# Optimization experiments

Measured on AMD Instinct MI355X. Metric: run time of the kernel, lower is better.

## Reference

```python
import jax, jax.numpy as jnp
import numpy as np

B, C, P, H, W = 64, 2048, 4, 14, 14
HID = C * P // 2  # 4096
S = H * W         # 196


def setup_inputs() -> dict:
    key = jax.random.key(0)
    k1, k2, k3, k4, k5 = jax.random.split(key, 5)
    x = jax.random.normal(k1, (B, C, H, W), dtype=jnp.float32)
    w1 = jax.random.normal(k2, (HID, C), dtype=jnp.float32) * 0.02
    b1 = jnp.zeros((HID,), dtype=jnp.float32)
    w2 = jax.random.normal(k3, (C * P, HID), dtype=jnp.float32) * 0.02
    b2 = jnp.zeros((C * P,), dtype=jnp.float32)
    return {"x": x, "w1": w1, "b1": b1, "w2": w2, "b2": b2}


def reference(x, w1, b1, w2, b2):
    # SE-style gating: global average pool -> fc1 -> sigmoid -> fc2 -> sigmoid
    g = x.mean(axis=(2, 3))                                  # [B, C]
    h = jax.nn.sigmoid(g @ w1.T + b1)                        # [B, HID]
    w = jax.nn.sigmoid(h @ w2.T + b2).reshape(B, P, C)       # grouping_result [B, P, C]
    # Weighted feature: mean over channels of w[b,p,c] * x[b,c,s].
    # Original materializes [B,P,C,196] then AdaptiveAvgPool3d over C;
    # mathematically this is a batched matmul divided by C.
    xs = x.reshape(B, C, S)                                  # [B, C, 196]
    feat = jnp.einsum('bpc,bcs->bps', w, xs) / C             # [B, P, 196]
    return (w, feat.reshape(B, P, H, W))
```

## Files before the change

kernel.cpp:

```cpp
#include <hip/hip_runtime.h>
#include <cstdint>
#include <cstddef>

typedef __attribute__((ext_vector_type(4))) float  f32x4;
typedef __attribute__((ext_vector_type(8))) short  short8;
typedef __attribute__((ext_vector_type(4))) short  short4v;

__device__ __forceinline__ short f2bf(float f) {
  unsigned u = __float_as_uint(f);
  u += 0x7FFF + ((u >> 16) & 1);
  return (short)(u >> 16);
}
__device__ __forceinline__ float sigmoidf(float x) {
  return 1.0f / (1.0f + __expf(-x));
}

__global__ __launch_bounds__(256) void pool_kernel(const float* __restrict__ x,
                                                   float* __restrict__ g,
                                                   int nrows) {
  int gid  = blockIdx.x * 256 + threadIdx.x;
  int row  = gid >> 6;
  int lane = threadIdx.x & 63;
  if (row >= nrows) return;
  float s = 0.f;
  if (lane < 49) {
    const float4* p = (const float4*)(x + (size_t)row * 196);
    float4 v = p[lane];
    s = v.x + v.y + v.z + v.w;
  }
#pragma unroll
  for (int off = 32; off > 0; off >>= 1) s += __shfl_down(s, off);
  if (lane == 0) g[row] = s * (1.0f / 196.0f);
}

template<int N, int K, int KCHUNK>
__global__ __launch_bounds__(256) void gemm_bt_part(const float* __restrict__ A,
                                                    const float* __restrict__ B,
                                                    float* __restrict__ part) {
  constexpr int BM = 64, BN = 64, BK = 64;
  constexpr int NT = N / BN;
  const int nt = blockIdx.x % NT;
  const int ks = blockIdx.x / NT;
  const int n0 = nt * BN;
  const int k0 = ks * KCHUNK;

  __shared__ short As[BM * BK];
  __shared__ short Bs[BN * BK];

  const int tid  = threadIdx.x;
  const int lane = tid & 63;
  const int wv   = tid >> 6;
  const int wm   = wv >> 1, wn = wv & 1;

  f32x4 acc[2][2] = {};

  for (int t = 0; t < KCHUNK / BK; ++t) {
    const int kt = k0 + t * BK;
    __syncthreads();
#pragma unroll
    for (int i = 0; i < 4; ++i) {
      int f = i * 256 + tid;
      int row = f >> 4, c4 = f & 15;
      float4 v = *(const float4*)(A + (size_t)row * K + kt + c4 * 4);
      short4v sv; sv.x = f2bf(v.x); sv.y = f2bf(v.y); sv.z = f2bf(v.z); sv.w = f2bf(v.w);
      int bo = (c4 * 8) ^ ((row & 7) << 4);
      *(short4v*)(As + row * 64 + (bo >> 1)) = sv;
    }
#pragma unroll
    for (int i = 0; i < 4; ++i) {
      int f = i * 256 + tid;
      int row = f >> 4, c4 = f & 15;
      float4 v = *(const float4*)(B + (size_t)(n0 + row) * K + kt + c4 * 4);
      short4v sv; sv.x = f2bf(v.x); sv.y = f2bf(v.y); sv.z = f2bf(v.z); sv.w = f2bf(v.w);
      int bo = (c4 * 8) ^ ((row & 7) << 4);
      *(short4v*)(Bs + row * 64 + (bo >> 1)) = sv;
    }
    __syncthreads();
#pragma unroll
    for (int kk = 0; kk < 2; ++kk) {
      const int kbyte = kk * 64 + ((lane >> 4) << 4);
      short8 af[2], bf[2];
#pragma unroll
      for (int mi = 0; mi < 2; ++mi) {
        int row = wm * 32 + mi * 16 + (lane & 15);
        int bo  = kbyte ^ ((row & 7) << 4);
        af[mi]  = *(const short8*)(As + row * 64 + (bo >> 1));
      }
#pragma unroll
      for (int ni = 0; ni < 2; ++ni) {
        int row = wn * 32 + ni * 16 + (lane & 15);
        int bo  = kbyte ^ ((row & 7) << 4);
        bf[ni]  = *(const short8*)(Bs + row * 64 + (bo >> 1));
      }
#pragma unroll
      for (int mi = 0; mi < 2; ++mi)
#pragma unroll
        for (int ni = 0; ni < 2; ++ni)
          acc[mi][ni] = __builtin_amdgcn_mfma_f32_16x16x32_bf16(af[mi], bf[ni], acc[mi][ni], 0, 0, 0);
    }
  }
  float* pp = part + (size_t)ks * BM * N;
#pragma unroll
  for (int mi = 0; mi < 2; ++mi)
#pragma unroll
    for (int ni = 0; ni < 2; ++ni)
#pragma unroll
      for (int r = 0; r < 4; ++r) {
        int m = wm * 32 + mi * 16 + ((lane >> 4) << 2) + r;
        int n = n0 + wn * 32 + ni * 16 + (lane & 15);
        pp[(size_t)m * N + n] = acc[mi][ni][r];
      }
}

template<int KS>
__global__ __launch_bounds__(256) void bias_sigmoid_reduce(const float* __restrict__ part,
                                                           const float* __restrict__ bias,
                                                           float* __restrict__ out,
                                                           int MN, int N) {
  int i = blockIdx.x * 256 + threadIdx.x;
  int e = i * 4;
  if (e >= MN) return;
  float4 s = {0.f, 0.f, 0.f, 0.f};
#pragma unroll
  for (int k = 0; k < KS; ++k) {
    float4 v = *(const float4*)(part + (size_t)k * MN + e);
    s.x += v.x; s.y += v.y; s.z += v.z; s.w += v.w;
  }
  float4 b = *(const float4*)(bias + (e % N));
  s.x = sigmoidf(s.x + b.x);
  s.y = sigmoidf(s.y + b.y);
  s.z = sigmoidf(s.z + b.z);
  s.w = sigmoidf(s.w + b.w);
  *(float4*)(out + e) = s;
}

__global__ __launch_bounds__(256) void einsum_fused(const float* __restrict__ x,
                                                    const float* __restrict__ part,
                                                    const float* __restrict__ b2,
                                                    float* __restrict__ wout,
                                                    float* __restrict__ fpart) {
  const int b  = blockIdx.x >> 4;
  const int cc = blockIdx.x & 15;
  __shared__ float gs[4 * 128];
  const int tid = threadIdx.x;
#pragma unroll
  for (int i = 0; i < 2; ++i) {
    int idx = i * 256 + tid;
    int p = idx >> 7, c = idx & 127;
    int n = p * 2048 + cc * 128 + c;
    float s = 0.f;
#pragma unroll
    for (int ks = 0; ks < 8; ++ks)
      s += part[(size_t)ks * 64 * 8192 + (size_t)b * 8192 + n];
    s = sigmoidf(s + b2[n]);
    wout[(size_t)b * 8192 + n] = s;
    gs[idx] = s;
  }
  __syncthreads();
  if (tid < 196) {
    const float* xp = x + (size_t)b * 2048 * 196 + (size_t)cc * 128 * 196 + tid;
    float a0 = 0, a1 = 0, a2 = 0, a3 = 0;
#pragma unroll 8
    for (int c = 0; c < 128; ++c) {
      float xv = xp[(size_t)c * 196];
      a0 += gs[c]        * xv;
      a1 += gs[128 + c]  * xv;
      a2 += gs[256 + c]  * xv;
      a3 += gs[384 + c]  * xv;
    }
    float* fp = fpart + ((size_t)(b * 16 + cc) * 4) * 196 + tid;
    fp[0]   = a0;
    fp[196] = a1;
    fp[392] = a2;
    fp[588] = a3;
  }
}

__global__ __launch_bounds__(256) void feat_reduce(const float* __restrict__ fpart,
                                                   float* __restrict__ feat) {
  int i = blockIdx.x * 256 + threadIdx.x;
  if (i >= 64 * 4 * 196) return;
  int s = i % 196;
  int p = (i / 196) & 3;
  int b = i / 784;
  float sum = 0.f;
#pragma unroll
  for (int cc = 0; cc < 16; ++cc)
    sum += fpart[((size_t)(b * 16 + cc) * 4 + p) * 196 + s];
  feat[i] = sum * (1.0f / 2048.0f);
}

extern "C" void kernel_launch(void* const* d_in, const int* in_sizes, int n_in,
                              void* d_out, int out_size, void* d_ws, size_t ws_size,
                              hipStream_t stream) {
  const float* x  = (const float*)d_in[0];
  const float* w1 = (const float*)d_in[1];
  const float* b1 = (const float*)d_in[2];
  const float* w2 = (const float*)d_in[3];
  const float* b2 = (const float*)d_in[4];
  float* out = (float*)d_out;

  float* g     = (float*)d_ws;
  float* h     = g + 64 * 2048;
  float* part  = h + 64 * 4096;
  float* fpart = part + 4194304;

  float* wout = out;
  float* feat = out + 524288;

  pool_kernel<<<(64 * 2048) / 4, 256, 0, stream>>>(x, g, 64 * 2048);

  gemm_bt_part<4096, 2048, 128><<<(4096 / 64) * 16, 256, 0, stream>>>(g, w1, part);
  bias_sigmoid_reduce<16><<<(64 * 4096 / 4) / 256, 256, 0, stream>>>(part, b1, h, 64 * 4096, 4096);

  gemm_bt_part<8192, 4096, 512><<<(8192 / 64) * 8, 256, 0, stream>>>(h, w2, part);

  einsum_fused<<<64 * 16, 256, 0, stream>>>(x, part, b2, wout, fpart);

  feat_reduce<<<(50176 + 255) / 256, 256, 0, stream>>>(fpart, feat);
}
```

Measured before the change: 108.9 us.

## Replace split-K GEMMs with in-block K-reduction and fused bias-sigmoid epilogue

Replaces the shared-memory-tiled split-K GEMMs, which wrote full partial-sum arrays to global memory, with a kernel in which each 512-thread block owns 16 output columns. Its 8 waves split K, run register-prefetched MFMAs that read weights straight from global, reduce through shared memory and apply bias plus sigmoid in place. This removes the separate bias/sigmoid reduce kernel and the large partial-sum round trips. Pooled and hidden activations are now stored as bf16 to halve their traffic, and the einsum kernel reads the finished gate weights instead of reducing partials. In exchange there is no LDS reuse of A across columns and each block launches larger.

Result: faster. 105.0 us (-3.6%).

```diff
diff --git a/kernel.cpp b/kernel.cpp
--- a/kernel.cpp
+++ b/kernel.cpp
@@ -4,7 +4,6 @@
 
 typedef __attribute__((ext_vector_type(4))) float  f32x4;
 typedef __attribute__((ext_vector_type(8))) short  short8;
-typedef __attribute__((ext_vector_type(4))) short  short4v;
 
 __device__ __forceinline__ short f2bf(float f) {
   unsigned u = __float_as_uint(f);
@@ -16,7 +15,7 @@
 }
 
 __global__ __launch_bounds__(256) void pool_kernel(const float* __restrict__ x,
-                                                   float* __restrict__ g,
+                                                   short* __restrict__ g,
                                                    int nrows) {
   int gid  = blockIdx.x * 256 + threadIdx.x;
   int row  = gid >> 6;
@@ -30,131 +29,102 @@
   }
 #pragma unroll
   for (int off = 32; off > 0; off >>= 1) s += __shfl_down(s, off);
-  if (lane == 0) g[row] = s * (1.0f / 196.0f);
+  if (lane == 0) g[row] = f2bf(s * (1.0f / 196.0f));
 }
 
-template<int N, int K, int KCHUNK>
-__global__ __launch_bounds__(256) void gemm_bt_part(const float* __restrict__ A,
-                                                    const float* __restrict__ B,
-                                                    float* __restrict__ part) {
-  constexpr int BM = 64, BN = 64, BK = 64;
-  constexpr int NT = N / BN;
-  const int nt = blockIdx.x % NT;
-  const int ks = blockIdx.x / NT;
-  const int n0 = nt * BN;
-  const int k0 = ks * KCHUNK;
+template<int N, int K, bool OUT_BF16>
+__global__ __launch_bounds__(512, 4) void gemm_fused(const short* __restrict__ A,
+                                                     const float* __restrict__ B,
+                                                     const float* __restrict__ bias,
+                                                     void* __restrict__ outp) {
+  constexpr int KW = K / 8;
+  constexpr int NK = KW / 32;
+  const int n0  = blockIdx.x * 16;
+  const int tid = threadIdx.x;
+  const int l   = tid & 63;
+  const int wv  = tid >> 6;
+  const int kw0 = wv * KW;
 
-  __shared__ short As[BM * BK];
-  __shared__ short Bs[BN * BK];
+  __shared__ float red[8 * 1024];
 
-  const int tid  = threadIdx.x;
-  const int lane = tid & 63;
-  const int wv   = tid >> 6;
-  const int wm   = wv >> 1, wn = wv & 1;
+  const int ko = (l >> 4) * 8;
+  const float* Bp = B + (size_t)(n0 + (l & 15)) * K + kw0 + ko;
+  const short* Ap = A + (size_t)(l & 15) * K + kw0 + ko;
 
-  f32x4 acc[2][2] = {};
+  f32x4 acc0 = {}, acc1 = {}, acc2 = {}, acc3 = {};
 
-  for (int t = 0; t < KCHUNK / BK; ++t) {
-    const int kt = k0 + t * BK;
-    __syncthreads();
+  float4 bc0 = *(const float4*)(Bp);
+  float4 bc1 = *(const float4*)(Bp + 4);
+  short8 ac0 = *(const short8*)(Ap);
+  short8 ac1 = *(const short8*)(Ap + 16 * K);
+  short8 ac2 = *(const short8*)(Ap + 32 * K);
+  short8 ac3 = *(const short8*)(Ap + 48 * K);
+
+  for (int t = 0; t < NK; ++t) {
+    float4 bn0 = {}, bn1 = {};
+    short8 an0 = {}, an1 = {}, an2 = {}, an3 = {};
+    if (t + 1 < NK) {
+      const float* bp = Bp + (t + 1) * 32;
+      const short* ap = Ap + (t + 1) * 32;
+      bn0 = *(const float4*)(bp);
+      bn1 = *(const float4*)(bp + 4);
+      an0 = *(const short8*)(ap);
+      an1 = *(const short8*)(ap + 16 * K);
+      an2 = *(const short8*)(ap + 32 * K);
+      an3 = *(const short8*)(ap + 48 * K);
+    }
+    short8 bb;
+    bb[0] = f2bf(bc0.x); bb[1] = f2bf(bc0.y); bb[2] = f2bf(bc0.z); bb[3] = f2bf(bc0.w);
+    bb[4] = f2bf(bc1.x); bb[5] = f2bf(bc1.y); bb[6] = f2bf(bc1.z); bb[7] = f2bf(bc1.w);
+    acc0 = __builtin_amdgcn_mfma_f32_16x16x32_bf16(ac0, bb, acc0, 0, 0, 0);
+    acc1 = __builtin_amdgcn_mfma_f32_16x16x32_bf16(ac1, bb, acc1, 0, 0, 0);
+    acc2 = __builtin_amdgcn_mfma_f32_16x16x32_bf16(ac2, bb, acc2, 0, 0, 0);
+    acc3 = __builtin_amdgcn_mfma_f32_16x16x32_bf16(ac3, bb, acc3, 0, 0, 0);
+    bc0 = bn0; bc1 = bn1;
+    ac0 = an0; ac1 = an1; ac2 = an2; ac3 = an3;
+  }
+
+  {
+    float* rw = red + wv * 1024;
+    const int mb = (l >> 4) << 2;
+    const int nn = l & 15;
 #pragma unroll
-    for (int i = 0; i < 4; ++i) {
-      int f = i * 256 + tid;
-      int row = f >> 4, c4 = f & 15;
-      float4 v = *(const float4*)(A + (size_t)row * K + kt + c4 * 4);
-      short4v sv; sv.x = f2bf(v.x); sv.y = f2bf(v.y); sv.z = f2bf(v.z); sv.w = f2bf(v.w);
-      int bo = (c4 * 8) ^ ((row & 7) << 4);
-      *(short4v*)(As + row * 64 + (bo >> 1)) = sv;
-    }
+    for (int r = 0; r < 4; ++r) rw[(0  + mb + r) * 16 + nn] = acc0[r];
 #pragma unroll
-    for (int i = 0; i < 4; ++i) {
-      int f = i * 256 + tid;
-      int row = f >> 4, c4 = f & 15;
-      float4 v = *(const float4*)(B + (size_t)(n0 + row) * K + kt + c4 * 4);
-      short4v sv; sv.x = f2bf(v.x); sv.y = f2bf(v.y); sv.z = f2bf(v.z); sv.w = f2bf(v.w);
-      int bo = (c4 * 8) ^ ((row & 7) << 4);
-      *(short4v*)(Bs + row * 64 + (bo >> 1)) = sv;
-    }
-    __syncthreads();
+    for (int r = 0; r < 4; ++r) rw[(16 + mb + r) * 16 + nn] = acc1[r];
 #pragma unroll
-    for (int kk = 0; kk < 2; ++kk) {
-      const int kbyte = kk * 64 + ((lane >> 4) << 4);
-      short8 af[2], bf[2];
+    for (int r = 0; r < 4; ++r) rw[(32 + mb + r) * 16 + nn] = acc2[r];
 #pragma unroll
-      for (int mi = 0; mi < 2; ++mi) {
-        int row = wm * 32 + mi * 16 + (lane & 15);
-        int bo  = kbyte ^ ((row & 7) << 4);
-        af[mi]  = *(const short8*)(As + row * 64 + (bo >> 1));
-      }
+    for (int r = 0; r < 4; ++r) rw[(48 + mb + r) * 16 + nn] = acc3[r];
+  }
+  __syncthreads();
+
 #pragma unroll
-      for (int ni = 0; ni < 2; ++ni) {
-        int row = wn * 32 + ni * 16 + (lane & 15);
-        int bo  = kbyte ^ ((row & 7) << 4);
-        bf[ni]  = *(const short8*)(Bs + row * 64 + (bo >> 1));
-      }
+  for (int i = tid; i < 1024; i += 512) {
+    float s = 0.f;
 #pragma unroll
-      for (int mi = 0; mi < 2; ++mi)
-#pragma unroll
-        for (int ni = 0; ni < 2; ++ni)
-          acc[mi][ni] = __builtin_amdgcn_mfma_f32_16x16x32_bf16(af[mi], bf[ni], acc[mi][ni], 0, 0, 0);
-    }
+    for (int w = 0; w < 8; ++w) s += red[w * 1024 + i];
+    int m  = i >> 4;
+    int nn = n0 + (i & 15);
+    s = sigmoidf(s + bias[nn]);
+    if constexpr (OUT_BF16) ((short*)outp)[(size_t)m * N + nn] = f2bf(s);
+    else                    ((float*)outp)[(size_t)m * N + nn] = s;
   }
-  float* pp = part + (size_t)ks * BM * N;
-#pragma unroll
-  for (int mi = 0; mi < 2; ++mi)
-#pragma unroll
-    for (int ni = 0; ni < 2; ++ni)
-#pragma unroll
-      for (int r = 0; r < 4; ++r) {
-        int m = wm * 32 + mi * 16 + ((lane >> 4) << 2) + r;
-        int n = n0 + wn * 32 + ni * 16 + (lane & 15);
-        pp[(size_t)m * N + n] = acc[mi][ni][r];
-      }
 }
 
-template<int KS>
-__global__ __launch_bounds__(256) void bias_sigmoid_reduce(const float* __restrict__ part,
-                                                           const float* __restrict__ bias,
-                                                           float* __restrict__ out,
-                                                           int MN, int N) {
-  int i = blockIdx.x * 256 + threadIdx.x;
-  int e = i * 4;
-  if (e >= MN) return;
-  float4 s = {0.f, 0.f, 0.f, 0.f};
-#pragma unroll
-  for (int k = 0; k < KS; ++k) {
-    float4 v = *(const float4*)(part + (size_t)k * MN + e);
-    s.x += v.x; s.y += v.y; s.z += v.z; s.w += v.w;
-  }
-  float4 b = *(const float4*)(bias + (e % N));
-  s.x = sigmoidf(s.x + b.x);
-  s.y = sigmoidf(s.y + b.y);
-  s.z = sigmoidf(s.z + b.z);
-  s.w = sigmoidf(s.w + b.w);
-  *(float4*)(out + e) = s;
-}
-
-__global__ __launch_bounds__(256) void einsum_fused(const float* __restrict__ x,
-                                                    const float* __restrict__ part,
-                                                    const float* __restrict__ b2,
-                                                    float* __restrict__ wout,
-                                                    float* __restrict__ fpart) {
+__global__ __launch_bounds__(256) void einsum_part(const float* __restrict__ x,
+                                                   const float* __restrict__ wg,
+                                                   float* __restrict__ fpart) {
   const int b  = blockIdx.x >> 4;
   const int cc = blockIdx.x & 15;
   __shared__ float gs[4 * 128];
   const int tid = threadIdx.x;
+  const float* wb = wg + (size_t)b * 8192 + cc * 128;
 #pragma unroll
   for (int i = 0; i < 2; ++i) {
     int idx = i * 256 + tid;
     int p = idx >> 7, c = idx & 127;
-    int n = p * 2048 + cc * 128 + c;
-    float s = 0.f;
-#pragma unroll
-    for (int ks = 0; ks < 8; ++ks)
-      s += part[(size_t)ks * 64 * 8192 + (size_t)b * 8192 + n];
-    s = sigmoidf(s + b2[n]);
-    wout[(size_t)b * 8192 + n] = s;
-    gs[idx] = s;
+    gs[idx] = wb[p * 2048 + c];
   }
   __syncthreads();
   if (tid < 196) {
@@ -163,10 +133,10 @@
 #pragma unroll 8
     for (int c = 0; c < 128; ++c) {
       float xv = xp[(size_t)c * 196];
-      a0 += gs[c]        * xv;
-      a1 += gs[128 + c]  * xv;
-      a2 += gs[256 + c]  * xv;
-      a3 += gs[384 + c]  * xv;
+      a0 += gs[c]       * xv;
+      a1 += gs[128 + c] * xv;
+      a2 += gs[256 + c] * xv;
+      a3 += gs[384 + c] * xv;
     }
     float* fp = fpart + ((size_t)(b * 16 + cc) * 4) * 196 + tid;
     fp[0]   = a0;
@@ -200,22 +170,20 @@
   const float* b2 = (const float*)d_in[4];
   float* out = (float*)d_out;
 
-  float* g     = (float*)d_ws;
-  float* h     = g + 64 * 2048;
-  float* part  = h + 64 * 4096;
-  float* fpart = part + 4194304;
+  short* g_bf  = (short*)d_ws;
+  short* h_bf  = g_bf + 64 * 2048;
+  float* fpart = (float*)((char*)d_ws + (1 << 20));
 
   float* wout = out;
   float* feat = out + 524288;
 
-  pool_kernel<<<(64 * 2048) / 4, 256, 0, stream>>>(x, g, 64 * 2048);
+  pool_kernel<<<(64 * 2048) / 4, 256, 0, stream>>>(x, g_bf, 64 * 2048);
 
-  gemm_bt_part<4096, 2048, 128><<<(4096 / 64) * 16, 256, 0, stream>>>(g, w1, part);
-  bias_sigmoid_reduce<16><<<(64 * 4096 / 4) / 256, 256, 0, stream>>>(part, b1, h, 64 * 4096, 4096);
+  gemm_fused<4096, 2048, true><<<4096 / 16, 512, 0, stream>>>(g_bf, w1, b1, h_bf);
 
-  gemm_bt_part<8192, 4096, 512><<<(8192 / 64) * 8, 256, 0, stream>>>(h, w2, part);
+  gemm_fused<8192, 4096, false><<<8192 / 16, 512, 0, stream>>>(h_bf, w2, b2, wout);
 
-  einsum_fused<<<64 * 16, 256, 0, stream>>>(x, part, b2, wout, fpart);
+  einsum_part<<<64 * 16, 256, 0, stream>>>(x, wout, fpart);
 
   feat_reduce<<<(50176 + 255) / 256, 256, 0, stream>>>(fpart, feat);
 }
```
